# Performance work log

Hardware: AMD Instinct MI355X
Metric: run time of the kernel (lower is better)

The kernel has to match this reference:

```python
import jax, jax.numpy as jnp
import numpy as np

N = 50000      # nodes
E = 800000     # edges
IN = 128       # in_channels
H = 128        # hidden_channels
OUT = 500      # out_channels
EPS = 1e-5


def setup_inputs() -> dict:
    key = jax.random.key(0)
    ks = jax.random.split(key, 8)
    def rn(k, shape, scale=0.05):
        return jax.random.normal(k, shape, jnp.float32) * scale
    return {
        "x": jax.random.normal(ks[0], (N, IN), jnp.float32),
        "edge_index": jax.random.randint(ks[1], (2, E), 0, N, dtype=jnp.int32),
        "W1": rn(ks[2], (IN, H)), "b1": jnp.zeros((H,), jnp.float32),
        "g1": jnp.ones((H,), jnp.float32), "be1": jnp.zeros((H,), jnp.float32),
        "W2": rn(ks[3], (H, 2 * H)), "b2": jnp.zeros((2 * H,), jnp.float32),
        "g2": jnp.ones((2 * H,), jnp.float32), "be2": jnp.zeros((2 * H,), jnp.float32),
        "W3": rn(ks[4], (2 * H, H)), "b3": jnp.zeros((H,), jnp.float32),
        "g3": jnp.ones((H,), jnp.float32), "be3": jnp.zeros((H,), jnp.float32),
        "Wl1": rn(ks[5], (H, H // 2)), "bl1": jnp.zeros((H // 2,), jnp.float32),
        "g4": jnp.ones((H // 2,), jnp.float32), "be4": jnp.zeros((H // 2,), jnp.float32),
        "Wl2": rn(ks[6], (H // 2, OUT)), "bl2": jnp.zeros((OUT,), jnp.float32),
    }


def layer_norm(x, g, b):
    mu = jnp.mean(x, axis=-1, keepdims=True)
    var = jnp.mean(jnp.square(x - mu), axis=-1, keepdims=True)
    return (x - mu) * jax.lax.rsqrt(var + EPS) * g + b


def gcn_conv(x, W, b, src, dst, n):
    # PyG GCNConv: x' = D^{-1/2} (A + I) D^{-1/2} (x W) + b, with self-loops.
    h = x @ W                                   # [N, F]
    ones = jnp.ones(src.shape[0], h.dtype)
    deg = jax.ops.segment_sum(ones, dst, num_segments=n) + 1.0  # +1 self-loop
    dinv = jnp.where(deg > 0, jax.lax.rsqrt(deg), 0.0)          # [N]
    coef = dinv[src] * dinv[dst]                # [E]
    agg = jax.ops.segment_sum(h[src] * coef[:, None], dst, num_segments=n)
    agg = agg + h * jnp.square(dinv)[:, None]   # self-loop messages
    return agg + b


def reference(x, edge_index, W1, b1, g1, be1, W2, b2, g2, be2,
              W3, b3, g3, be3, Wl1, bl1, g4, be4, Wl2, bl2):
    # eval mode: dropout is identity
    src, dst = edge_index[0], edge_index[1]
    n = x.shape[0]
    h = jax.nn.elu(layer_norm(gcn_conv(x, W1, b1, src, dst, n), g1, be1))
    h = jax.nn.elu(layer_norm(gcn_conv(h, W2, b2, src, dst, n), g2, be2))
    h = jax.nn.elu(layer_norm(gcn_conv(h, W3, b3, src, dst, n), g3, be3))
    h = jax.nn.elu(layer_norm(h @ Wl1 + bl1, g4, be4))
    return h @ Wl2 + bl2
```

## Files before the change

kernel.cpp:

```cpp
#include <hip/hip_runtime.h>
#include <cstdint>


#define LN_EPS 1e-5f

typedef __attribute__((ext_vector_type(8))) short bf16x8;
typedef __attribute__((ext_vector_type(4))) float f32x4;

static __device__ __forceinline__ ushort f2bf(float f) {
  union { float f; uint u; } c; c.f = f;
  uint u = c.u;
  return (ushort)((u + 0x7fffu + ((u >> 16) & 1u)) >> 16);
}
static __device__ __forceinline__ float bf2f(ushort h) {
  union { uint u; float f; } c; c.u = (uint)h << 16;
  return c.f;
}


__global__ void deg_kernel(const int* __restrict__ dst, int* __restrict__ deg, int E) {
  int e = blockIdx.x * blockDim.x + threadIdx.x;
  if (e < E) atomicAdd(&deg[dst[e]], 1);
}

__global__ void scan1_kernel(const int* __restrict__ deg, int* __restrict__ excl,
                             int* __restrict__ bsums, float* __restrict__ dinv, int N) {
  __shared__ int s[256];
  int tid = threadIdx.x;
  int i = blockIdx.x * 256 + tid;
  int v = (i < N) ? deg[i] : 0;
  s[tid] = v;
  __syncthreads();
  for (int o = 1; o < 256; o <<= 1) {
    int t = (tid >= o) ? s[tid - o] : 0;
    __syncthreads();
    if (tid >= o) s[tid] += t;
    __syncthreads();
  }
  if (i < N) {
    excl[i] = s[tid] - v;
    dinv[i] = rsqrtf((float)v + 1.0f);
  }
  if (tid == 255) bsums[blockIdx.x] = s[tid];
}

__global__ void scan23_kernel(int* __restrict__ rowptr, int* __restrict__ fill,
                              const int* __restrict__ bsums, int N, int Etotal, int nb) {
  __shared__ int sh[256];
  const int tid = threadIdx.x;
  const int bix = blockIdx.x;
  int v = (tid < bix && tid < nb) ? bsums[tid] : 0;
  sh[tid] = v;
  __syncthreads();
  for (int o = 128; o > 0; o >>= 1) {
    if (tid < o) sh[tid] += sh[tid + o];
    __syncthreads();
  }
  const int off = sh[0];
  int i = bix * 256 + tid;
  if (i < N) {
    int r = rowptr[i] + off;
    rowptr[i] = r;
    fill[i] = r;
  } else if (i == N) {
    rowptr[N] = Etotal;
  }
}

__global__ void fill_kernel(const int* __restrict__ src, const int* __restrict__ dst,
                            int* __restrict__ fill, int* __restrict__ srcs, int E) {
  int e = blockIdx.x * blockDim.x + threadIdx.x;
  if (e >= E) return;
  int idx = atomicAdd(&fill[dst[e]], 1);
  srcs[idx] = src[e];
}


struct WConvArgs {
  const float* w[5];
  ushort* wt[5];
  int K[5], N[5];
  int off[6];
};

__global__ void prep_kernel(WConvArgs a, int total, int* __restrict__ deg, int Nn) {
  int i = blockIdx.x * blockDim.x + threadIdx.x;
  if (i < Nn) deg[i] = 0;
  if (i < 768) a.wt[4][32000 + i] = 0;
  if (i >= total) return;
  int m = 0;
  while (i >= a.off[m + 1]) m++;
  int j = i - a.off[m];
  int k = j / a.N[m], n = j - k * a.N[m];
  a.wt[m][(size_t)n * a.K[m] + k] = f2bf(a.w[m][j]);
}

#define TBM 128
#define TBN 128
#define TBK 32
#define LDK 40

template <int AF32>
__global__ __launch_bounds__(256, 2) void mfma_gemm_kernel(
    const void* __restrict__ A, const ushort* __restrict__ Bt,
    const float* __restrict__ bias, ushort* __restrict__ Cout,
    int M, int N, int K) {
  __shared__ ushort As[TBM][LDK];
  __shared__ ushort Bs[TBN][LDK];
  const int tid = threadIdx.x;
  const int lane = tid & 63;
  const int w = tid >> 6;
  const int wm = w & 1, wn = w >> 1;
  const int quad = lane >> 4, l16 = lane & 15;
  const int rowBase = blockIdx.y * TBM;
  const int colBase = blockIdx.x * TBN;

  f32x4 acc[4][4] = {};
  const int lr = tid >> 2;
  const int lk = (tid & 3) * 8;

  for (int k0 = 0; k0 < K; k0 += TBK) {
#pragma unroll
    for (int h = 0; h < 2; h++) {
      int r = lr + h * 64;
      int grow = rowBase + r;
      if (AF32) {
        const float* Af = (const float*)A;
        float4 v0 = make_float4(0.f, 0.f, 0.f, 0.f), v1 = v0;
        if (grow < M) {
          const float* ap = Af + (size_t)grow * K + k0 + lk;
          v0 = *(const float4*)ap;
          v1 = *(const float4*)(ap + 4);
        }
        uint4 wv;
        wv.x = (uint)f2bf(v0.x) | ((uint)f2bf(v0.y) << 16);
        wv.y = (uint)f2bf(v0.z) | ((uint)f2bf(v0.w) << 16);
        wv.z = (uint)f2bf(v1.x) | ((uint)f2bf(v1.y) << 16);
        wv.w = (uint)f2bf(v1.z) | ((uint)f2bf(v1.w) << 16);
        *(uint4*)&As[r][lk] = wv;
      } else {
        const ushort* Ab = (const ushort*)A;
        uint4 va = make_uint4(0, 0, 0, 0);
        if (grow < M) va = *(const uint4*)(Ab + (size_t)grow * K + k0 + lk);
        *(uint4*)&As[r][lk] = va;
      }
      int gcol = colBase + r;
      uint4 vb = make_uint4(0, 0, 0, 0);
      if (gcol < N) vb = *(const uint4*)(Bt + (size_t)gcol * K + k0 + lk);
      *(uint4*)&Bs[r][lk] = vb;
    }
    __syncthreads();
    bf16x8 af[4], bfr[4];
#pragma unroll
    for (int i = 0; i < 4; i++) {
      af[i]  = *(const bf16x8*)&As[wm * 64 + i * 16 + l16][quad * 8];
      bfr[i] = *(const bf16x8*)&Bs[wn * 64 + i * 16 + l16][quad * 8];
    }
#pragma unroll
    for (int i = 0; i < 4; i++)
#pragma unroll
      for (int j = 0; j < 4; j++)
        acc[i][j] = __builtin_amdgcn_mfma_f32_16x16x32_bf16(af[i], bfr[j], acc[i][j], 0, 0, 0);
    __syncthreads();
  }
#pragma unroll
  for (int i = 0; i < 4; i++) {
    int row0 = rowBase + wm * 64 + i * 16 + quad * 4;
#pragma unroll
    for (int j = 0; j < 4; j++) {
      int col = colBase + wn * 64 + j * 16 + l16;
      if (col >= N) continue;
      float bv = bias ? bias[col] : 0.f;
#pragma unroll
      for (int r = 0; r < 4; r++) {
        int row = row0 + r;
        if (row >= M) continue;
        Cout[(size_t)row * N + col] = f2bf(acc[i][j][r] + bv);
      }
    }
  }
}

__global__ __launch_bounds__(256) void l45_kernel(
    const ushort* __restrict__ A, const ushort* __restrict__ Bt1,
    const float* __restrict__ bias1, const float* __restrict__ gamma,
    const float* __restrict__ beta, const ushort* __restrict__ Bt2,
    const float* __restrict__ bias2, float* __restrict__ Cout, int M) {
  __shared__ ushort h4s[64][68];
  __shared__ __align__(16) float sout[16][500];
  const int tid = threadIdx.x;
  const int lane = tid & 63;
  const int w = tid >> 6;
  const int quad = lane >> 4, l16 = lane & 15;
  const int rowBase = blockIdx.x * 64;
  const int waveRow = rowBase + w * 16;

  bf16x8 bfr1[4][4];
#pragma unroll
  for (int j = 0; j < 4; j++)
#pragma unroll
    for (int kk = 0; kk < 4; kk++)
      bfr1[j][kk] = *(const bf16x8*)(Bt1 + (size_t)(j * 16 + l16) * 128 + kk * 32 + quad * 8);

  const int arow = waveRow + l16;
  bf16x8 af[4] = {};
  if (arow < M) {
#pragma unroll
    for (int kk = 0; kk < 4; kk++)
      af[kk] = *(const bf16x8*)(A + (size_t)arow * 128 + kk * 32 + quad * 8);
  }

  f32x4 acc1[4] = {};
#pragma unroll
  for (int j = 0; j < 4; j++)
#pragma unroll
    for (int kk = 0; kk < 4; kk++)
      acc1[j] = __builtin_amdgcn_mfma_f32_16x16x32_bf16(af[kk], bfr1[j][kk], acc1[j], 0, 0, 0);

#pragma unroll
  for (int r = 0; r < 4; r++) {
    float v[4];
    float s = 0.f;
#pragma unroll
    for (int j = 0; j < 4; j++) {
      v[j] = acc1[j][r] + bias1[j * 16 + l16];
      s += v[j];
    }
#pragma unroll
    for (int o = 8; o >= 1; o >>= 1) s += __shfl_xor(s, o, 16);
    float mean = s * (1.0f / 64.0f);
    float q = 0.f;
#pragma unroll
    for (int j = 0; j < 4; j++) {
      float d = v[j] - mean;
      q += d * d;
    }
#pragma unroll
    for (int o = 8; o >= 1; o >>= 1) q += __shfl_xor(q, o, 16);
    float rstd = rsqrtf(q * (1.0f / 64.0f) + LN_EPS);
    int lrow = w * 16 + quad * 4 + r;
#pragma unroll
    for (int j = 0; j < 4; j++) {
      int col = j * 16 + l16;
      float y = (v[j] - mean) * rstd * gamma[col] + beta[col];
      y = (y > 0.f) ? y : expm1f(y);
      h4s[lrow][col] = f2bf(y);
    }
  }

  bf16x8 breg[8][2];
  float bvreg[8];
#pragma unroll
  for (int c = 0; c < 8; c++) {
    const int bcol = (w * 8 + c) * 16 + l16;
    breg[c][0] = *(const bf16x8*)(Bt2 + (size_t)bcol * 64 + quad * 8);
    breg[c][1] = *(const bf16x8*)(Bt2 + (size_t)bcol * 64 + 32 + quad * 8);
    bvreg[c] = (bcol < 500) ? bias2[bcol] : 0.f;
  }
  __syncthreads();

#pragma unroll 1
  for (int rt = 0; rt < 4; rt++) {
    bf16x8 a0 = *(const bf16x8*)&h4s[rt * 16 + l16][quad * 8];
    bf16x8 a1 = *(const bf16x8*)&h4s[rt * 16 + l16][quad * 8 + 32];
#pragma unroll
    for (int c = 0; c < 8; c++) {
      f32x4 pacc = {0.f, 0.f, 0.f, 0.f};
      pacc = __builtin_amdgcn_mfma_f32_16x16x32_bf16(a0, breg[c][0], pacc, 0, 0, 0);
      pacc = __builtin_amdgcn_mfma_f32_16x16x32_bf16(a1, breg[c][1], pacc, 0, 0, 0);
      const int col = (w * 8 + c) * 16 + l16;
      if (col < 500) {
#pragma unroll
        for (int r = 0; r < 4; r++)
          sout[quad * 4 + r][col] = pacc[r] + bvreg[c];
      }
    }
    __syncthreads();
#pragma unroll
    for (int k = 0; k < 8; k++) {
      int idx = k * 256 + tid;
      if (idx < 2000) {
        int r = idx / 125;
        int c4 = idx - r * 125;
        int grow = rowBase + rt * 16 + r;
        if (grow < M) {
          float4 v = *(float4*)&sout[r][c4 * 4];
          *(float4*)&Cout[(size_t)grow * 500 + c4 * 4] = v;
        }
      }
    }
    __syncthreads();
  }
}


static __device__ __forceinline__ void acc8(float* a, uint4 v, float c) {
  a[0] += c * bf2f((ushort)(v.x & 0xffffu)); a[1] += c * bf2f((ushort)(v.x >> 16));
  a[2] += c * bf2f((ushort)(v.y & 0xffffu)); a[3] += c * bf2f((ushort)(v.y >> 16));
  a[4] += c * bf2f((ushort)(v.z & 0xffffu)); a[5] += c * bf2f((ushort)(v.z >> 16));
  a[6] += c * bf2f((ushort)(v.w & 0xffffu)); a[7] += c * bf2f((ushort)(v.w >> 16));
}

__global__ __launch_bounds__(256) void agg_kernel(
    const ushort* __restrict__ hb, const int* __restrict__ rowptr,
    const int* __restrict__ srcs, const float* __restrict__ dinv,
    uint* __restrict__ out, int Nn) {
  const int wave = threadIdx.x >> 6;
  const int n = blockIdx.x * 4 + wave;
  if (n >= Nn) return;
  const int lane = threadIdx.x & 63;
  const int g = lane >> 4, l16 = lane & 15;
  const uint4* h4 = (const uint4*)hb;
  const float di = dinv[n];
  float a[8] = {0.f, 0.f, 0.f, 0.f, 0.f, 0.f, 0.f, 0.f};
  if (g == 0) {
    uint4 sv = h4[(size_t)n * 16 + l16];
    acc8(a, sv, di * di);
  }
  int i = rowptr[n] + g;
  const int e = rowptr[n + 1];
  for (; i + 4 < e; i += 8) {
    int s0 = srcs[i], s1 = srcs[i + 4];
    float c0 = dinv[s0] * di, c1 = dinv[s1] * di;
    uint4 v0 = h4[(size_t)s0 * 16 + l16];
    uint4 v1 = h4[(size_t)s1 * 16 + l16];
    acc8(a, v0, c0);
    acc8(a, v1, c1);
  }
  if (i < e) {
    int s = srcs[i];
    float c = dinv[s] * di;
    uint4 v = h4[(size_t)s * 16 + l16];
    acc8(a, v, c);
  }
#pragma unroll
  for (int k = 0; k < 8; k++) {
    a[k] += __shfl_xor(a[k], 16);
    a[k] += __shfl_xor(a[k], 32);
  }
  if (g == 0) {
    uint4 o;
    o.x = (uint)f2bf(a[0]) | ((uint)f2bf(a[1]) << 16);
    o.y = (uint)f2bf(a[2]) | ((uint)f2bf(a[3]) << 16);
    o.z = (uint)f2bf(a[4]) | ((uint)f2bf(a[5]) << 16);
    o.w = (uint)f2bf(a[6]) | ((uint)f2bf(a[7]) << 16);
    ((uint4*)out)[(size_t)n * 16 + l16] = o;
  }
}

__global__ __launch_bounds__(256) void agg_ln_kernel(
    const ushort* __restrict__ hb, const int* __restrict__ rowptr,
    const int* __restrict__ srcs, const float* __restrict__ dinv,
    const float* __restrict__ bias, const float* __restrict__ gamma,
    const float* __restrict__ beta, uint* __restrict__ out, int Nn) {
  const int wave = threadIdx.x >> 6;
  const int n = blockIdx.x * 4 + wave;
  if (n >= Nn) return;
  const int lane = threadIdx.x & 63;
  const int g = lane >> 4, l16 = lane & 15;
  const uint4* h4 = (const uint4*)hb;
  const float di = dinv[n];
  float a[8] = {0.f, 0.f, 0.f, 0.f, 0.f, 0.f, 0.f, 0.f};
  if (g == 0) {
    uint4 sv = h4[(size_t)n * 16 + l16];
    acc8(a, sv, di * di);
    float4 b0 = ((const float4*)bias)[l16 * 2];
    float4 b1 = ((const float4*)bias)[l16 * 2 + 1];
    a[0] += b0.x; a[1] += b0.y; a[2] += b0.z; a[3] += b0.w;
    a[4] += b1.x; a[5] += b1.y; a[6] += b1.z; a[7] += b1.w;
  }
  int i = rowptr[n] + g;
  const int e = rowptr[n + 1];
  for (; i + 4 < e; i += 8) {
    int s0 = srcs[i], s1 = srcs[i + 4];
    float c0 = dinv[s0] * di, c1 = dinv[s1] * di;
    uint4 v0 = h4[(size_t)s0 * 16 + l16];
    uint4 v1 = h4[(size_t)s1 * 16 + l16];
    acc8(a, v0, c0);
    acc8(a, v1, c1);
  }
  if (i < e) {
    int s = srcs[i];
    float c = dinv[s] * di;
    uint4 v = h4[(size_t)s * 16 + l16];
    acc8(a, v, c);
  }
#pragma unroll
  for (int k = 0; k < 8; k++) {
    a[k] += __shfl_xor(a[k], 16);
    a[k] += __shfl_xor(a[k], 32);
  }
  float s = ((a[0] + a[1]) + (a[2] + a[3])) + ((a[4] + a[5]) + (a[6] + a[7]));
  s += __shfl_xor(s, 8);
  s += __shfl_xor(s, 4);
  s += __shfl_xor(s, 2);
  s += __shfl_xor(s, 1);
  float mean = s * (1.0f / 128.0f);
  float q = 0.f;
#pragma unroll
  for (int k = 0; k < 8; k++) {
    float d = a[k] - mean;
    q += d * d;
  }
  q += __shfl_xor(q, 8);
  q += __shfl_xor(q, 4);
  q += __shfl_xor(q, 2);
  q += __shfl_xor(q, 1);
  float rstd = rsqrtf(q * (1.0f / 128.0f) + LN_EPS);
  if (g == 0) {
    float4 g0 = ((const float4*)gamma)[l16 * 2];
    float4 g1 = ((const float4*)gamma)[l16 * 2 + 1];
    float4 e0 = ((const float4*)beta)[l16 * 2];
    float4 e1 = ((const float4*)beta)[l16 * 2 + 1];
    float gv[8] = {g0.x, g0.y, g0.z, g0.w, g1.x, g1.y, g1.z, g1.w};
    float ev[8] = {e0.x, e0.y, e0.z, e0.w, e1.x, e1.y, e1.z, e1.w};
    float y[8];
#pragma unroll
    for (int k = 0; k < 8; k++) {
      float t = (a[k] - mean) * rstd * gv[k] + ev[k];
      y[k] = (t > 0.f) ? t : expm1f(t);
    }
    uint4 o;
    o.x = (uint)f2bf(y[0]) | ((uint)f2bf(y[1]) << 16);
    o.y = (uint)f2bf(y[2]) | ((uint)f2bf(y[3]) << 16);
    o.z = (uint)f2bf(y[4]) | ((uint)f2bf(y[5]) << 16);
    o.w = (uint)f2bf(y[6]) | ((uint)f2bf(y[7]) << 16);
    ((uint4*)out)[(size_t)n * 16 + l16] = o;
  }
}

template <int F, bool IN_BF16>
__global__ __launch_bounds__(F) void ln_elu_kernel(const void* __restrict__ xin,
                                                   const float* __restrict__ g,
                                                   const float* __restrict__ be,
                                                   ushort* __restrict__ out) {
  constexpr int NW = (F + 63) / 64;
  __shared__ float sb[NW];
  const int row = blockIdx.x;
  const int f = threadIdx.x;
  float v;
  if (IN_BF16) v = bf2f(((const ushort*)xin)[(size_t)row * F + f]);
  else         v = ((const float*)xin)[(size_t)row * F + f];
  float s = v;
#pragma unroll
  for (int o = 32; o >= 1; o >>= 1) s += __shfl_xor(s, o);
  float mean;
  if constexpr (NW == 1) {
    mean = s * (1.0f / F);
  } else {
    if ((f & 63) == 0) sb[f >> 6] = s;
    __syncthreads();
    float t = 0.f;
#pragma unroll
    for (int w2 = 0; w2 < NW; w2++) t += sb[w2];
    mean = t * (1.0f / F);
    __syncthreads();
  }
  float d = v - mean;
  float q = d * d;
#pragma unroll
  for (int o = 32; o >= 1; o >>= 1) q += __shfl_xor(q, o);
  float var;
  if constexpr (NW == 1) {
    var = q * (1.0f / F);
  } else {
    if ((f & 63) == 0) sb[f >> 6] = q;
    __syncthreads();
    float t = 0.f;
#pragma unroll
    for (int w2 = 0; w2 < NW; w2++) t += sb[w2];
    var = t * (1.0f / F);
  }
  float y = d * rsqrtf(var + LN_EPS) * g[f] + be[f];
  out[(size_t)row * F + f] = f2bf((y > 0.f) ? y : expm1f(y));
}


extern "C" void kernel_launch(void* const* d_in, const int* in_sizes, int n_in,
                              void* d_out, int out_size, void* d_ws, size_t ws_size,
                              hipStream_t stream) {
  const float* x   = (const float*)d_in[0];
  const int*   ei  = (const int*)d_in[1];
  const float* W1  = (const float*)d_in[2];
  const float* b1  = (const float*)d_in[3];
  const float* g1  = (const float*)d_in[4];
  const float* be1 = (const float*)d_in[5];
  const float* W2  = (const float*)d_in[6];
  const float* b2  = (const float*)d_in[7];
  const float* g2  = (const float*)d_in[8];
  const float* be2 = (const float*)d_in[9];
  const float* W3  = (const float*)d_in[10];
  const float* b3  = (const float*)d_in[11];
  const float* g3  = (const float*)d_in[12];
  const float* be3 = (const float*)d_in[13];
  const float* Wl1 = (const float*)d_in[14];
  const float* bl1 = (const float*)d_in[15];
  const float* g4  = (const float*)d_in[16];
  const float* be4 = (const float*)d_in[17];
  const float* Wl2 = (const float*)d_in[18];
  const float* bl2 = (const float*)d_in[19];

  const int N = in_sizes[0] / 128;
  const int E = in_sizes[1] / 2;
  const int* esrc = ei;
  const int* edst = ei + E;

  char* p = (char*)d_ws;
  ushort* Pb = (ushort*)p;            p += (size_t)N * 256 * 2;
  ushort* Qb = (ushort*)p;            p += (size_t)N * 256 * 2;
  ushort* W1t = (ushort*)p;           p += 128 * 128 * 2;
  ushort* W2t = (ushort*)p;           p += 128 * 256 * 2;
  ushort* W3t = (ushort*)p;           p += 256 * 128 * 2;
  ushort* Wl1t = (ushort*)p;          p += 128 * 64 * 2;
  ushort* Wl2t = (ushort*)p;          p += 64 * 512 * 2;
  int*   srcs  = (int*)p;             p += (size_t)E * 4;
  int*   deg   = (int*)p;             p += (size_t)N * 4;
  float* dinv  = (float*)p;           p += (size_t)N * 4;
  int*   rowptr= (int*)p;             p += (size_t)(N + 2) * 4;
  int*   fill  = (int*)p;             p += (size_t)N * 4;
  int*   bsums = (int*)p;             p += 256 * 4;

  const int nb = (N + 255) / 256;
  const int eb = (E + 255) / 256;

  WConvArgs wa;
  wa.w[0] = W1;  wa.wt[0] = W1t;  wa.K[0] = 128; wa.N[0] = 128;
  wa.w[1] = W2;  wa.wt[1] = W2t;  wa.K[1] = 128; wa.N[1] = 256;
  wa.w[2] = W3;  wa.wt[2] = W3t;  wa.K[2] = 256; wa.N[2] = 128;
  wa.w[3] = Wl1; wa.wt[3] = Wl1t; wa.K[3] = 128; wa.N[3] = 64;
  wa.w[4] = Wl2; wa.wt[4] = Wl2t; wa.K[4] = 64;  wa.N[4] = 500;
  wa.off[0] = 0;
  for (int m = 0; m < 5; m++) wa.off[m + 1] = wa.off[m] + wa.K[m] * wa.N[m];
  int wtotal = wa.off[5];
  int ptotal = wtotal > N ? wtotal : N;
  prep_kernel<<<(ptotal + 255) / 256, 256, 0, stream>>>(wa, wtotal, deg, N);

  deg_kernel<<<eb, 256, 0, stream>>>(edst, deg, E);
  scan1_kernel<<<nb, 256, 0, stream>>>(deg, rowptr, bsums, dinv, N);
  scan23_kernel<<<(N + 256) / 256, 256, 0, stream>>>(rowptr, fill, bsums, N, E, nb);
  fill_kernel<<<eb, 256, 0, stream>>>(esrc, edst, fill, srcs, E);

  const int ab = (N + 3) / 4;
  auto grid_of = [&](int M, int Nn) {
    return dim3((Nn + TBN - 1) / TBN, (M + TBM - 1) / TBM);
  };

  mfma_gemm_kernel<1><<<grid_of(N, 128), 256, 0, stream>>>(
      x, W1t, nullptr, Pb, N, 128, 128);
  agg_ln_kernel<<<ab, 256, 0, stream>>>(Pb, rowptr, srcs, dinv, b1, g1, be1, (uint*)Qb, N);

  agg_kernel<<<ab, 256, 0, stream>>>(Qb, rowptr, srcs, dinv, (uint*)Pb, N);
  mfma_gemm_kernel<0><<<grid_of(N, 256), 256, 0, stream>>>(
      Pb, W2t, b2, Qb, N, 256, 128);
  ln_elu_kernel<256, true><<<N, 256, 0, stream>>>(Qb, g2, be2, Pb);

  mfma_gemm_kernel<0><<<grid_of(N, 128), 256, 0, stream>>>(
      Pb, W3t, nullptr, Qb, N, 128, 256);
  agg_ln_kernel<<<ab, 256, 0, stream>>>(Qb, rowptr, srcs, dinv, b3, g3, be3, (uint*)Pb, N);

  l45_kernel<<<dim3((N + 63) / 64), 256, 0, stream>>>(
      Pb, Wl1t, bl1, g4, be4, Wl2t, bl2, (float*)d_out, N);
}
```

Baseline: 497.1 us.

## Fuse layer-2 aggregation, GEMM, and LayerNorm+ELU into one kernel

Replaces three launches for layer 2 (edge aggregation, MFMA GEMM with bias, LN+ELU) with one kernel. Each 512-thread block aggregates 128 node rows into LDS as bf16, runs a 128x256 MFMA GEMM reading W2t from global memory, then applies bias, LayerNorm and ELU in registers before writing. This removes the round trips of the aggregated and pre-norm intermediates through HBM, along with two launches. In exchange, each block fetches W2t directly from global without LDS staging, does the gather serially over 16 iterations per wave, and stores outputs as scattered 2-byte writes.

```diff
diff --git a/kernel.cpp b/kernel.cpp
--- a/kernel.cpp
+++ b/kernel.cpp
@@ -181,6 +181,118 @@
   }
 }
 
+
+static __device__ __forceinline__ void acc8(float* a, uint4 v, float c) {
+  a[0] += c * bf2f((ushort)(v.x & 0xffffu)); a[1] += c * bf2f((ushort)(v.x >> 16));
+  a[2] += c * bf2f((ushort)(v.y & 0xffffu)); a[3] += c * bf2f((ushort)(v.y >> 16));
+  a[4] += c * bf2f((ushort)(v.z & 0xffffu)); a[5] += c * bf2f((ushort)(v.z >> 16));
+  a[6] += c * bf2f((ushort)(v.w & 0xffffu)); a[7] += c * bf2f((ushort)(v.w >> 16));
+}
+
+__global__ __launch_bounds__(512) void l2_kernel(
+    const ushort* __restrict__ Hin, const int* __restrict__ rowptr,
+    const int* __restrict__ srcs, const float* __restrict__ dinv,
+    const ushort* __restrict__ W2t, const float* __restrict__ bias,
+    const float* __restrict__ gamma, const float* __restrict__ beta,
+    ushort* __restrict__ Hout, int M) {
+  __shared__ ushort As[128][136];
+  const int tid = threadIdx.x;
+  const int lane = tid & 63;
+  const int w = tid >> 6;
+  const int g = lane >> 4, l16 = lane & 15;
+  const int rowBase = blockIdx.x * 128;
+
+  const uint4* h4 = (const uint4*)Hin;
+  for (int it = 0; it < 16; ++it) {
+    const int lrow = it * 8 + w;
+    const int n = rowBase + lrow;
+    if (n < M) {
+      const float di = dinv[n];
+      float a[8] = {0.f, 0.f, 0.f, 0.f, 0.f, 0.f, 0.f, 0.f};
+      if (g == 0) {
+        uint4 sv = h4[(size_t)n * 16 + l16];
+        acc8(a, sv, di * di);
+      }
+      int i = rowptr[n] + g;
+      const int e = rowptr[n + 1];
+      for (; i + 4 < e; i += 8) {
+        int s0 = srcs[i], s1 = srcs[i + 4];
+        float c0 = dinv[s0] * di, c1 = dinv[s1] * di;
+        uint4 v0 = h4[(size_t)s0 * 16 + l16];
+        uint4 v1 = h4[(size_t)s1 * 16 + l16];
+        acc8(a, v0, c0);
+        acc8(a, v1, c1);
+      }
+      if (i < e) {
+        int s = srcs[i];
+        float c = dinv[s] * di;
+        uint4 v = h4[(size_t)s * 16 + l16];
+        acc8(a, v, c);
+      }
+#pragma unroll
+      for (int k = 0; k < 8; k++) {
+        a[k] += __shfl_xor(a[k], 16);
+        a[k] += __shfl_xor(a[k], 32);
+      }
+      if (g == 0) {
+        uint4 o;
+        o.x = (uint)f2bf(a[0]) | ((uint)f2bf(a[1]) << 16);
+        o.y = (uint)f2bf(a[2]) | ((uint)f2bf(a[3]) << 16);
+        o.z = (uint)f2bf(a[4]) | ((uint)f2bf(a[5]) << 16);
+        o.w = (uint)f2bf(a[6]) | ((uint)f2bf(a[7]) << 16);
+        *(uint4*)&As[lrow][l16 * 8] = o;
+      }
+    }
+  }
+  __syncthreads();
+
+  const int quad = g;
+  const int wrow = w * 16;
+  f32x4 acc[16] = {};
+#pragma unroll
+  for (int k0 = 0; k0 < 128; k0 += 32) {
+    bf16x8 af = *(const bf16x8*)&As[wrow + l16][k0 + quad * 8];
+#pragma unroll
+    for (int j = 0; j < 16; j++) {
+      bf16x8 bf = *(const bf16x8*)(W2t + (size_t)(j * 16 + l16) * 128 + k0 + quad * 8);
+      acc[j] = __builtin_amdgcn_mfma_f32_16x16x32_bf16(af, bf, acc[j], 0, 0, 0);
+    }
+  }
+
+#pragma unroll
+  for (int r = 0; r < 4; r++) {
+    float v[16];
+    float s = 0.f;
+#pragma unroll
+    for (int j = 0; j < 16; j++) {
+      v[j] = acc[j][r] + bias[j * 16 + l16];
+      s += v[j];
+    }
+#pragma unroll
+    for (int o = 8; o >= 1; o >>= 1) s += __shfl_xor(s, o, 16);
+    float mean = s * (1.0f / 256.0f);
+    float q = 0.f;
+#pragma unroll
+    for (int j = 0; j < 16; j++) {
+      float d = v[j] - mean;
+      q += d * d;
+    }
+#pragma unroll
+    for (int o = 8; o >= 1; o >>= 1) q += __shfl_xor(q, o, 16);
+    float rstd = rsqrtf(q * (1.0f / 256.0f) + LN_EPS);
+    int grow = rowBase + wrow + quad * 4 + r;
+    if (grow < M) {
+#pragma unroll
+      for (int j = 0; j < 16; j++) {
+        int col = j * 16 + l16;
+        float y = (v[j] - mean) * rstd * gamma[col] + beta[col];
+        y = (y > 0.f) ? y : expm1f(y);
+        Hout[(size_t)grow * 256 + col] = f2bf(y);
+      }
+    }
+  }
+}
+
 __global__ __launch_bounds__(256) void l45_kernel(
     const ushort* __restrict__ A, const ushort* __restrict__ Bt1,
     const float* __restrict__ bias1, const float* __restrict__ gamma,
@@ -290,61 +402,6 @@
       }
     }
     __syncthreads();
-  }
-}
-
-
-static __device__ __forceinline__ void acc8(float* a, uint4 v, float c) {
-  a[0] += c * bf2f((ushort)(v.x & 0xffffu)); a[1] += c * bf2f((ushort)(v.x >> 16));
-  a[2] += c * bf2f((ushort)(v.y & 0xffffu)); a[3] += c * bf2f((ushort)(v.y >> 16));
-  a[4] += c * bf2f((ushort)(v.z & 0xffffu)); a[5] += c * bf2f((ushort)(v.z >> 16));
-  a[6] += c * bf2f((ushort)(v.w & 0xffffu)); a[7] += c * bf2f((ushort)(v.w >> 16));
-}
-
-__global__ __launch_bounds__(256) void agg_kernel(
-    const ushort* __restrict__ hb, const int* __restrict__ rowptr,
-    const int* __restrict__ srcs, const float* __restrict__ dinv,
-    uint* __restrict__ out, int Nn) {
-  const int wave = threadIdx.x >> 6;
-  const int n = blockIdx.x * 4 + wave;
-  if (n >= Nn) return;
-  const int lane = threadIdx.x & 63;
-  const int g = lane >> 4, l16 = lane & 15;
-  const uint4* h4 = (const uint4*)hb;
-  const float di = dinv[n];
-  float a[8] = {0.f, 0.f, 0.f, 0.f, 0.f, 0.f, 0.f, 0.f};
-  if (g == 0) {
-    uint4 sv = h4[(size_t)n * 16 + l16];
-    acc8(a, sv, di * di);
-  }
-  int i = rowptr[n] + g;
-  const int e = rowptr[n + 1];
-  for (; i + 4 < e; i += 8) {
-    int s0 = srcs[i], s1 = srcs[i + 4];
-    float c0 = dinv[s0] * di, c1 = dinv[s1] * di;
-    uint4 v0 = h4[(size_t)s0 * 16 + l16];
-    uint4 v1 = h4[(size_t)s1 * 16 + l16];
-    acc8(a, v0, c0);
-    acc8(a, v1, c1);
-  }
-  if (i < e) {
-    int s = srcs[i];
-    float c = dinv[s] * di;
-    uint4 v = h4[(size_t)s * 16 + l16];
-    acc8(a, v, c);
-  }
-#pragma unroll
-  for (int k = 0; k < 8; k++) {
-    a[k] += __shfl_xor(a[k], 16);
-    a[k] += __shfl_xor(a[k], 32);
-  }
-  if (g == 0) {
-    uint4 o;
-    o.x = (uint)f2bf(a[0]) | ((uint)f2bf(a[1]) << 16);
-    o.y = (uint)f2bf(a[2]) | ((uint)f2bf(a[3]) << 16);
-    o.z = (uint)f2bf(a[4]) | ((uint)f2bf(a[5]) << 16);
-    o.w = (uint)f2bf(a[6]) | ((uint)f2bf(a[7]) << 16);
-    ((uint4*)out)[(size_t)n * 16 + l16] = o;
   }
 }
 
@@ -427,52 +484,6 @@
     o.w = (uint)f2bf(y[6]) | ((uint)f2bf(y[7]) << 16);
     ((uint4*)out)[(size_t)n * 16 + l16] = o;
   }
-}
-
-template <int F, bool IN_BF16>
-__global__ __launch_bounds__(F) void ln_elu_kernel(const void* __restrict__ xin,
-                                                   const float* __restrict__ g,
-                                                   const float* __restrict__ be,
-                                                   ushort* __restrict__ out) {
-  constexpr int NW = (F + 63) / 64;
-  __shared__ float sb[NW];
-  const int row = blockIdx.x;
-  const int f = threadIdx.x;
-  float v;
-  if (IN_BF16) v = bf2f(((const ushort*)xin)[(size_t)row * F + f]);
-  else         v = ((const float*)xin)[(size_t)row * F + f];
-  float s = v;
-#pragma unroll
-  for (int o = 32; o >= 1; o >>= 1) s += __shfl_xor(s, o);
-  float mean;
-  if constexpr (NW == 1) {
-    mean = s * (1.0f / F);
-  } else {
-    if ((f & 63) == 0) sb[f >> 6] = s;
-    __syncthreads();
-    float t = 0.f;
-#pragma unroll
-    for (int w2 = 0; w2 < NW; w2++) t += sb[w2];
-    mean = t * (1.0f / F);
-    __syncthreads();
-  }
-  float d = v - mean;
-  float q = d * d;
-#pragma unroll
-  for (int o = 32; o >= 1; o >>= 1) q += __shfl_xor(q, o);
-  float var;
-  if constexpr (NW == 1) {
-    var = q * (1.0f / F);
-  } else {
-    if ((f & 63) == 0) sb[f >> 6] = q;
-    __syncthreads();
-    float t = 0.f;
-#pragma unroll
-    for (int w2 = 0; w2 < NW; w2++) t += sb[w2];
-    var = t * (1.0f / F);
-  }
-  float y = d * rsqrtf(var + LN_EPS) * g[f] + be[f];
-  out[(size_t)row * F + f] = f2bf((y > 0.f) ? y : expm1f(y));
 }
 
 
@@ -549,10 +560,8 @@
       x, W1t, nullptr, Pb, N, 128, 128);
   agg_ln_kernel<<<ab, 256, 0, stream>>>(Pb, rowptr, srcs, dinv, b1, g1, be1, (uint*)Qb, N);
 
-  agg_kernel<<<ab, 256, 0, stream>>>(Qb, rowptr, srcs, dinv, (uint*)Pb, N);
-  mfma_gemm_kernel<0><<<grid_of(N, 256), 256, 0, stream>>>(
-      Pb, W2t, b2, Qb, N, 256, 128);
-  ln_elu_kernel<256, true><<<N, 256, 0, stream>>>(Qb, g2, be2, Pb);
+  l2_kernel<<<dim3((N + 127) / 128), 512, 0, stream>>>(
+      Qb, rowptr, srcs, dinv, W2t, b2, g2, be2, Pb, N);
 
   mfma_gemm_kernel<0><<<grid_of(N, 128), 256, 0, stream>>>(
       Pb, W3t, nullptr, Qb, N, 128, 256);
```

After: 571.7 us. 15.0% more time.
